# Optimization experiments

Hardware: AMD Instinct MI355X
Metric: run time of the kernel (lower is better)

The kernel has to match this reference:

```python
import jax, jax.numpy as jnp
import numpy as np

K = 10          # n_near
BN_EPS = 1e-5   # BatchNorm eps; running stats at init: mean=0, var=1


def knn_idx(xt, k):
    # xt: [b, n, c] -> [b, n, k] indices of k nearest (incl. self)
    sq = jnp.sum(xt * xt, axis=-1)                               # [b, n]
    d = sq[:, :, None] - 2.0 * jnp.einsum('bnc,bmc->bnm', xt, xt) + sq[:, None, :]
    return jax.lax.top_k(-d, k)[1]                               # [b, n, k]


def graph_feature(x, k):
    # x: [b, c, n] -> [b, 2c, n, k]  (DGCNN edge features)
    xt = x.transpose(0, 2, 1)                                    # [b, n, c]
    idx = knn_idx(xt, k)                                         # [b, n, k]
    nei = jnp.take_along_axis(xt[:, None, :, :], idx[..., None], axis=2)  # [b, n, k, c]
    cen = xt[:, :, None, :]                                      # [b, n, 1, c]
    feat = jnp.concatenate([nei - cen, jnp.broadcast_to(cen, nei.shape)], axis=-1)
    return feat.transpose(0, 3, 1, 2)                            # [b, 2c, n, k]


def conv_bn_act(x, w, b, g, t):
    # 1x1 conv (any spatial rank) + inference BatchNorm (mean=0, var=1) + GELU
    sh = (1, -1) + (1,) * (x.ndim - 2)
    y = jnp.einsum('oi,bi...->bo...', w, x) + b.reshape(sh)
    y = y * (g.reshape(sh) / jnp.sqrt(1.0 + BN_EPS)) + t.reshape(sh)
    return jax.nn.gelu(y)


def setup_inputs() -> dict:
    key = jax.random.key(0)
    ks = jax.random.split(key, 8)
    d = {'x': jax.random.normal(ks[0], (8, 64, 2048), jnp.float32)}
    dims = {'11': (152, 128), '12': (181, 152), '21': (430, 362),
            '22': (512, 430), '31': (595, 693), '32': (512, 595)}
    for i, (tag, (o, inp)) in enumerate(dims.items()):
        d['w' + tag] = jax.random.normal(jax.random.fold_in(key, i + 1), (o, inp), jnp.float32) * 0.02
        d['b' + tag] = jnp.zeros((o,), jnp.float32)
        d['g' + tag] = jnp.ones((o,), jnp.float32)
        d['t' + tag] = jnp.zeros((o,), jnp.float32)
    return d


def reference(x, w11, b11, g11, t11, w12, b12, g12, t12,
              w21, b21, g21, t21, w22, b22, g22, t22,
              w31, b31, g31, t31, w32, b32, g32, t32):
    f = graph_feature(x, K)                       # [b, 128, n, k]
    f = conv_bn_act(f, w11, b11, g11, t11)
    f = conv_bn_act(f, w12, b12, g12, t12)        # [b, 181, n, k]
    x1 = jnp.max(f, axis=-1)                      # [b, 181, n]
    f = graph_feature(x1, K)                      # [b, 362, n, k]
    f = conv_bn_act(f, w21, b21, g21, t21)
    f = conv_bn_act(f, w22, b22, g22, t22)        # [b, 512, n, k]
    x2 = jnp.max(f, axis=-1)                      # [b, 512, n]
    f = jnp.concatenate([x1, x2], axis=1)         # [b, 693, n]
    f = conv_bn_act(f, w31, b31, g31, t31)
    f = conv_bn_act(f, w32, b32, g32, t32)        # [b, 512, n]
    return f
```

## Files before the change

### kernel.cpp

```cpp
#include <hip/hip_runtime.h>


typedef float f4 __attribute__((ext_vector_type(4)));
typedef float f32x4 __attribute__((ext_vector_type(4)));
typedef short bf16x8 __attribute__((ext_vector_type(8)));

#define BNRSQ 0.9999950000374997f

__device__ __forceinline__ float gelu_f(float x){
  float a = 0.7978845608028654f * (x + 0.044715f * x * x * x);
  float e = __expf(2.0f * a);
  float t = 1.0f - 2.0f / (e + 1.0f);
  return 0.5f * x * (1.0f + t);
}

__device__ __forceinline__ short f2b(float x){
  unsigned u = __float_as_uint(x);
  unsigned r = (u + 0x7fffu + ((u >> 16) & 1u)) >> 16;
  return (short)r;
}
__device__ __forceinline__ float b2f(short s){
  return __uint_as_float(((unsigned)(unsigned short)s) << 16);
}

__global__ void makewt_k(const float* __restrict__ W, float* __restrict__ dst,
                         int O, int Cin, int Cpad, int ld, int split){
  int id = blockIdx.x * 256 + threadIdx.x;
  if (id >= Cpad * O) return;
  int c = id / O;
  int o = id - c * O;
  float v = 0.f;
  if (c < Cin){
    float w0 = W[(size_t)o * ld + c];
    v = split ? (W[(size_t)o * ld + Cin + c] - w0) : w0;
  }
  dst[id] = v;
}

__global__ void makew12r_k(const float* __restrict__ w12, float* __restrict__ Wr){
  int id = blockIdx.x * 256 + threadIdx.x;
  if (id >= 38 * 192 * 4) return;
  int i = id & 3;
  int c = (id >> 2) % 192;
  int kq = id / 768;
  int k = kq * 4 + i;
  float v = 0.f;
  if (c < 181 && k < 152) v = w12[(size_t)c * 152 + k];
  Wr[id] = v;
}

__global__ void makewsb_k(const float* __restrict__ W, short* __restrict__ dst){
  int n = blockIdx.x;
  int k = threadIdx.x;
  if (k >= 192) return;
  short v = 0;
  if (k < 181){
    if (n < 430) v = f2b(W[(size_t)n * 362 + k]);
    else if (n >= 448 && n < 878){
      int m = n - 448;
      v = f2b(W[(size_t)m * 362 + 181 + k] - W[(size_t)m * 362 + k]);
    }
  }
  dst[(size_t)n * 192 + k] = v;
}

__global__ void makewb_k(const float* __restrict__ W, short* __restrict__ dst,
                         int N, int K, int Kpad){
  int n = blockIdx.y;
  int k = blockIdx.x * 256 + threadIdx.x;
  if (k >= Kpad) return;
  short v = 0;
  if (n < N && k < K) v = f2b(W[(size_t)n * K + k]);
  dst[(size_t)n * Kpad + k] = v;
}

__global__ __launch_bounds__(256) void transpose_k(const float* __restrict__ x, float* __restrict__ xt){
  __shared__ float tile[64][65];
  int b = blockIdx.y;
  int n0 = blockIdx.x * 64;
  int t = threadIdx.x;
  int a = t & 63, r = t >> 6;
  #pragma unroll
  for (int s = 0; s < 16; s++){
    int c = r + s * 4;
    tile[c][a] = x[((size_t)b * 64 + c) * 2048 + n0 + a];
  }
  __syncthreads();
  #pragma unroll
  for (int s = 0; s < 16; s++){
    int n = r + s * 4;
    xt[((size_t)b * 2048 + n0 + n) * 64 + a] = tile[a][n];
  }
}

__global__ __launch_bounds__(256) void sqnorm_k(const float* __restrict__ X, float* __restrict__ sq,
                                                int C, int ld, int npts){
  int gid = blockIdx.x * blockDim.x + threadIdx.x;
  int wid = gid >> 6, lane = gid & 63;
  if (wid >= npts) return;
  const float* row = X + (size_t)wid * ld;
  float s = 0.f;
  for (int c = lane; c < C; c += 64){ float v = row[c]; s += v * v; }
  #pragma unroll
  for (int off = 32; off; off >>= 1) s += __shfl_xor(s, off);
  if (lane == 0) sq[wid] = s;
}

__global__ __launch_bounds__(256) void dist_k(const float* __restrict__ X, const float* __restrict__ sq,
                                              float* __restrict__ dist, int C, int ldx){
  __shared__ float As[16][132];
  __shared__ float Bs[16][132];
  const int z = blockIdx.z;
  const float* Xb = X + (size_t)z * 2048 * ldx;
  const float* sqb = sq + (z << 11);
  float* db = dist + (size_t)z * 2048 * 2048;
  const int i0 = blockIdx.y * 128, j0 = blockIdx.x * 128;
  const int t = threadIdx.x;
  const int ti = t >> 4, tj = t & 15;
  const int r = t & 127, q8 = (t >> 7) * 8;
  float acc[2][2][4][4];
  #pragma unroll
  for (int a = 0; a < 2; a++)
    #pragma unroll
    for (int b = 0; b < 2; b++)
      #pragma unroll
      for (int u = 0; u < 4; u++)
        #pragma unroll
        for (int v = 0; v < 4; v++) acc[a][b][u][v] = 0.f;
  const float* Ag = Xb + (size_t)(i0 + r) * ldx + q8;
  const float* Bg = Xb + (size_t)(j0 + r) * ldx + q8;
  for (int c0 = 0; c0 < C; c0 += 16){
    f4 av0 = *(const f4*)(Ag + c0);
    f4 av1 = *(const f4*)(Ag + c0 + 4);
    f4 bv0 = *(const f4*)(Bg + c0);
    f4 bv1 = *(const f4*)(Bg + c0 + 4);
    __syncthreads();
    #pragma unroll
    for (int i = 0; i < 4; i++){
      As[q8 + i][r] = av0[i];  As[q8 + 4 + i][r] = av1[i];
      Bs[q8 + i][r] = bv0[i];  Bs[q8 + 4 + i][r] = bv1[i];
    }
    __syncthreads();
    #pragma unroll
    for (int k = 0; k < 16; k++){
      f4 a0 = *(const f4*)&As[k][ti * 4];
      f4 a1 = *(const f4*)&As[k][ti * 4 + 64];
      f4 b0 = *(const f4*)&Bs[k][tj * 4];
      f4 b1 = *(const f4*)&Bs[k][tj * 4 + 64];
      #pragma unroll
      for (int u = 0; u < 4; u++)
        #pragma unroll
        for (int v = 0; v < 4; v++){
          acc[0][0][u][v] += a0[u] * b0[v];
          acc[0][1][u][v] += a0[u] * b1[v];
          acc[1][0][u][v] += a1[u] * b0[v];
          acc[1][1][u][v] += a1[u] * b1[v];
        }
    }
  }
  #pragma unroll
  for (int ia = 0; ia < 2; ia++){
    #pragma unroll
    for (int u = 0; u < 4; u++){
      int i = i0 + ia * 64 + ti * 4 + u;
      float si = sqb[i];
      #pragma unroll
      for (int jb = 0; jb < 2; jb++){
        int j = j0 + jb * 64 + tj * 4;
        f4 o;
        #pragma unroll
        for (int v = 0; v < 4; v++) o[v] = si + sqb[j + v] - 2.0f * acc[ia][jb][u][v];
        *(f4*)&db[(size_t)i * 2048 + j] = o;
      }
    }
  }
}

__global__ __launch_bounds__(256) void topk_k(const float* __restrict__ dist, int* __restrict__ idxout){
  int z = blockIdx.y;
  int lane = threadIdx.x & 63;
  int row = blockIdx.x * 4 + (threadIdx.x >> 6);
  const float* d = dist + (size_t)z * 2048 * 2048 + (size_t)row * 2048;
  float v[32];
  #pragma unroll
  for (int s = 0; s < 32; s++) v[s] = d[s * 64 + lane];
  int* outp = idxout + (size_t)z * 20480 + (size_t)row * 10;
  for (int it = 0; it < 10; ++it){
    float bv = 3.0e38f; int bi = 0x7fffffff;
    #pragma unroll
    for (int s = 0; s < 32; s++){
      if (v[s] < bv){ bv = v[s]; bi = s * 64 + lane; }
    }
    #pragma unroll
    for (int off = 32; off; off >>= 1){
      float ov = __shfl_xor(bv, off);
      int   oi = __shfl_xor(bi, off);
      if (ov < bv || (ov == bv && oi < bi)){ bv = ov; bi = oi; }
    }
    #pragma unroll
    for (int s = 0; s < 32; s++) if (s * 64 + lane == bi) v[s] = 3.0e38f;
    if (lane == 0) outp[it] = bi;
  }
}

__global__ __launch_bounds__(256) void yz_k(const float* __restrict__ Amat, int C,
                                            const float* __restrict__ B1, const float* __restrict__ B2,
                                            int O, float* __restrict__ Y, float* __restrict__ Z){
  __shared__ float As[16][68];
  __shared__ float B1s[16][68];
  __shared__ float B2s[16][68];
  int m0 = blockIdx.y * 64, o0 = blockIdx.x * 64;
  int t = threadIdx.x;
  int cc = t & 15, rr = t >> 4;
  int oo = t & 63, kk = t >> 6;
  float accY[4][4], accZ[4][4];
  #pragma unroll
  for (int u = 0; u < 4; u++)
    #pragma unroll
    for (int v = 0; v < 4; v++){ accY[u][v] = 0.f; accZ[u][v] = 0.f; }
  for (int c0 = 0; c0 < C; c0 += 16){
    #pragma unroll
    for (int u = 0; u < 4; u++){
      int ii = rr + u * 16;
      As[cc][ii] = ((c0 + cc) < C) ? Amat[(size_t)(m0 + ii) * C + c0 + cc] : 0.f;
    }
    #pragma unroll
    for (int u = 0; u < 4; u++){
      int c = kk * 4 + u;
      bool ok = ((c0 + c) < C) && ((o0 + oo) < O);
      B1s[c][oo] = ok ? B1[(size_t)(c0 + c) * O + o0 + oo] : 0.f;
      B2s[c][oo] = ok ? B2[(size_t)(c0 + c) * O + o0 + oo] : 0.f;
    }
    __syncthreads();
    #pragma unroll
    for (int k = 0; k < 16; k++){
      f4 a  = *(const f4*)&As[k][rr * 4];
      f4 b1 = *(const f4*)&B1s[k][cc * 4];
      f4 b2 = *(const f4*)&B2s[k][cc * 4];
      #pragma unroll
      for (int u = 0; u < 4; u++)
        #pragma unroll
        for (int v = 0; v < 4; v++){
          accY[u][v] += a[u] * b1[v];
          accZ[u][v] += a[u] * b2[v];
        }
    }
    __syncthreads();
  }
  #pragma unroll
  for (int u = 0; u < 4; u++){
    int m = m0 + rr * 4 + u;
    #pragma unroll
    for (int v = 0; v < 4; v++){
      int o = o0 + cc * 4 + v;
      if (o < O){
        Y[(size_t)m * O + o] = accY[u][v];
        Z[(size_t)m * O + o] = accZ[u][v];
      }
    }
  }
}

__global__ __launch_bounds__(256) void fused1_k(
    const float* __restrict__ Y1, const float* __restrict__ Z1,
    const int* __restrict__ idx, const float* __restrict__ Wr12,
    const float* __restrict__ bb11, const float* __restrict__ gg11, const float* __restrict__ tt11,
    const float* __restrict__ bb12, const float* __restrict__ gg12, const float* __restrict__ tt12,
    float* __restrict__ x1t){
  __shared__ float h1[80][152];
  __shared__ int sidx[80];
  const int n0 = blockIdx.x * 8;
  const int t = threadIdx.x;
  if (t < 80) sidx[t] = idx[(size_t)n0 * 10 + t];
  __syncthreads();
  const int base = (n0 >> 11) << 11;
  {
    const int tc = t & 63, tr = t >> 6;
    for (int c = tc; c < 152; c += 64){
      float bb = bb11[c], sc = gg11[c] * BNRSQ, tb = tt11[c];
      for (int r = tr; r < 80; r += 4){
        int p = r / 10;
        int j = base + sidx[r];
        float y = Y1[(size_t)j * 152 + c] + Z1[(size_t)(n0 + p) * 152 + c];
        h1[r][c] = gelu_f((y + bb) * sc + tb);
      }
    }
  }
  __syncthreads();
  const int p = t >> 5, kh = (t >> 4) & 1, cg = t & 15;
  const int rbase = p * 10 + kh * 5;
  float acc[5][12];
  #pragma unroll
  for (int k = 0; k < 5; k++)
    #pragma unroll
    for (int j = 0; j < 12; j++) acc[k][j] = 0.f;
  for (int kq = 0; kq < 38; kq++){
    const float* wp = Wr12 + ((size_t)kq * 192 + cg) * 4;
    f4 wv[12];
    #pragma unroll
    for (int j = 0; j < 12; j++) wv[j] = *(const f4*)(wp + j * 64);
    f4 hv[5];
    #pragma unroll
    for (int k = 0; k < 5; k++) hv[k] = *(const f4*)&h1[rbase + k][kq * 4];
    #pragma unroll
    for (int k = 0; k < 5; k++)
      #pragma unroll
      for (int j = 0; j < 12; j++)
        acc[k][j] += hv[k][0] * wv[j][0] + hv[k][1] * wv[j][1]
                   + hv[k][2] * wv[j][2] + hv[k][3] * wv[j][3];
  }
  #pragma unroll
  for (int j = 0; j < 12; j++){
    int c = cg + j * 16;
    float m = 0.f;
    if (c < 181){
      float bb = bb12[c], sc = gg12[c] * BNRSQ, tb = tt12[c];
      m = -3.0e38f;
      #pragma unroll
      for (int k = 0; k < 5; k++){
        float v = gelu_f((acc[k][j] + bb) * sc + tb);
        m = fmaxf(m, v);
      }
    }
    float o = __shfl_xor(m, 16);
    m = fmaxf(m, o);
    if (kh == 0) x1t[(size_t)(n0 + p) * 192 + c] = (c < 181) ? m : 0.f;
  }
}

__global__ __launch_bounds__(256) void castx1_k(const float* __restrict__ x1t, short* __restrict__ x1b){
  int id = blockIdx.x * 256 + threadIdx.x;
  f4 v = *(const f4*)&x1t[(size_t)id * 4];
  short4 o;
  o.x = f2b(v[0]); o.y = f2b(v[1]); o.z = f2b(v[2]); o.w = f2b(v[3]);
  *(short4*)&x1b[(size_t)id * 4] = o;
}

__global__ __launch_bounds__(256) void h2_k(
    const float* __restrict__ YZ, const int* __restrict__ idx,
    const float* __restrict__ bb21, const float* __restrict__ gg21, const float* __restrict__ tt21,
    short* __restrict__ H2){
  __shared__ int sidx[10];
  int p = blockIdx.x;
  int t = threadIdx.x;
  if (t < 10) sidx[t] = idx[(size_t)p * 10 + t];
  __syncthreads();
  int cA = t;
  int cB = t + 256;
  float zA = YZ[(size_t)p * 896 + 448 + cA] + bb21[cA];
  float scA = gg21[cA] * BNRSQ, tbA = tt21[cA];
  float zB = 0.f, scB = 0.f, tbB = 0.f;
  bool realB = cB < 430, padB = cB < 448;
  if (realB){
    zB = YZ[(size_t)p * 896 + 448 + cB] + bb21[cB];
    scB = gg21[cB] * BNRSQ; tbB = tt21[cB];
  }
  #pragma unroll
  for (int k = 0; k < 10; k++){
    int nb = sidx[k];
    size_t rb = ((size_t)p * 10 + k) * 448;
    float yA = YZ[(size_t)nb * 896 + cA] + zA;
    H2[rb + cA] = f2b(gelu_f(yA * scA + tbA));
    if (padB){
      short v = 0;
      if (realB){
        float yB = YZ[(size_t)nb * 896 + cB] + zB;
        v = f2b(gelu_f(yB * scB + tbB));
      }
      H2[rb + cB] = v;
    }
  }
}

template<int MODE>
__global__ __launch_bounds__(256) void gemm_k(const short* __restrict__ A,
                                              const short* __restrict__ Bt,
                                              int Kp, int Nld, int Nreal,
                                              const float* __restrict__ bv,
                                              const float* __restrict__ gv,
                                              const float* __restrict__ tv,
                                              void* __restrict__ outp){
  __shared__ short As[128][40];
  __shared__ short Bs[128][40];
  const int t = threadIdx.x;
  const int w = t >> 6, l = t & 63;
  const int m0 = blockIdx.y * 128, n0 = blockIdx.x * 128;
  f32x4 acc[2][8];
  #pragma unroll
  for (int i = 0; i < 2; i++)
    #pragma unroll
    for (int j = 0; j < 8; j++) acc[i][j] = (f32x4)0.f;
  const int ar = t >> 2, akc = t & 3;
  const short* Ag0 = A + (size_t)(m0 + ar) * Kp + akc * 8;
  const short* Ag1 = A + (size_t)(m0 + 64 + ar) * Kp + akc * 8;
  const short* Bg0 = Bt + (size_t)(n0 + ar) * Kp + akc * 8;
  const short* Bg1 = Bt + (size_t)(n0 + 64 + ar) * Kp + akc * 8;
  const int mrow = w * 32 + (l & 15);
  const int kg = (l >> 4) * 8;
  const int cl = l & 15;
  for (int k0 = 0; k0 < Kp; k0 += 32){
    int4 va0 = *(const int4*)(Ag0 + k0);
    int4 va1 = *(const int4*)(Ag1 + k0);
    int4 vb0 = *(const int4*)(Bg0 + k0);
    int4 vb1 = *(const int4*)(Bg1 + k0);
    __syncthreads();
    *(int4*)&As[ar][akc * 8]      = va0;
    *(int4*)&As[ar + 64][akc * 8] = va1;
    *(int4*)&Bs[ar][akc * 8]      = vb0;
    *(int4*)&Bs[ar + 64][akc * 8] = vb1;
    __syncthreads();
    bf16x8 a0 = *(const bf16x8*)&As[mrow][kg];
    bf16x8 a1 = *(const bf16x8*)&As[mrow + 16][kg];
    #pragma unroll
    for (int ni = 0; ni < 8; ni++){
      bf16x8 b = *(const bf16x8*)&Bs[cl + ni * 16][kg];
      acc[0][ni] = __builtin_amdgcn_mfma_f32_16x16x32_bf16(a0, b, acc[0][ni], 0, 0, 0);
      acc[1][ni] = __builtin_amdgcn_mfma_f32_16x16x32_bf16(a1, b, acc[1][ni], 0, 0, 0);
    }
  }
  const int rbase = (l >> 4) * 4;
  #pragma unroll
  for (int ni = 0; ni < 8; ni++){
    int n = n0 + ni * 16 + cl;
    float bb = 0.f, sc = 0.f, tb = 0.f;
    if (MODE != 2 && n < Nreal){ bb = bv[n]; sc = gv[n] * BNRSQ; tb = tv[n]; }
    #pragma unroll
    for (int mi = 0; mi < 2; mi++){
      #pragma unroll
      for (int r = 0; r < 4; r++){
        int m = m0 + w * 32 + mi * 16 + rbase + r;
        float a = acc[mi][ni][r];
        float v = (MODE == 2) ? a : gelu_f((a + bb) * sc + tb);
        if (MODE == 0) ((short*)outp)[(size_t)m * Nld + n] = f2b(v);
        else           ((float*)outp)[(size_t)m * Nld + n] = v;
      }
    }
  }
}

__global__ __launch_bounds__(256) void kmax_k(const short* __restrict__ Pb, float* __restrict__ x2t){
  int p = blockIdx.x;
  int t = threadIdx.x;
  #pragma unroll
  for (int j = 0; j < 2; j++){
    int o = t + j * 256;
    float m = -3.0e38f;
    #pragma unroll
    for (int k = 0; k < 10; k++) m = fmaxf(m, b2f(Pb[((size_t)p * 10 + k) * 512 + o]));
    x2t[(size_t)p * 512 + o] = m;
  }
}

__global__ __launch_bounds__(256) void fcat_k(const float* __restrict__ x1t, const float* __restrict__ x2t,
                                              short* __restrict__ F){
  size_t g = blockIdx.x;
  int t = threadIdx.x;
  for (int c = t; c < 704; c += 256){
    short v = 0;
    if (c < 181) v = f2b(x1t[g * 192 + c]);
    else if (c < 693) v = f2b(x2t[g * 512 + (c - 181)]);
    F[g * 704 + c] = v;
  }
}

__global__ __launch_bounds__(256) void trout_k(const float* __restrict__ H6, float* __restrict__ out){
  __shared__ float tile[64][65];
  int b = blockIdx.z;
  int nc = blockIdx.x * 64, oc = blockIdx.y * 64;
  int t = threadIdx.x;
  int a = t & 63, r = t >> 6;
  #pragma unroll
  for (int s = 0; s < 16; s++){
    int nl = r + s * 4;
    tile[nl][a] = H6[((size_t)b * 2048 + nc + nl) * 512 + oc + a];
  }
  __syncthreads();
  #pragma unroll
  for (int s = 0; s < 16; s++){
    int ol = r + s * 4;
    out[((size_t)(b * 512 + oc + ol)) * 2048 + nc + a] = tile[a][ol];
  }
}

extern "C" void kernel_launch(void* const* d_in, const int* in_sizes, int n_in,
                              void* d_out, int out_size, void* d_ws, size_t ws_size,
                              hipStream_t stream) {
  const float* x   = (const float*)d_in[0];
  const float* w11 = (const float*)d_in[1];
  const float* b11 = (const float*)d_in[2];
  const float* g11 = (const float*)d_in[3];
  const float* t11 = (const float*)d_in[4];
  const float* w12 = (const float*)d_in[5];
  const float* b12 = (const float*)d_in[6];
  const float* g12 = (const float*)d_in[7];
  const float* t12 = (const float*)d_in[8];
  const float* w21 = (const float*)d_in[9];
  const float* b21 = (const float*)d_in[10];
  const float* g21 = (const float*)d_in[11];
  const float* t21 = (const float*)d_in[12];
  const float* w22 = (const float*)d_in[13];
  const float* b22 = (const float*)d_in[14];
  const float* g22 = (const float*)d_in[15];
  const float* t22 = (const float*)d_in[16];
  const float* w31 = (const float*)d_in[17];
  const float* b31 = (const float*)d_in[18];
  const float* g31 = (const float*)d_in[19];
  const float* t31 = (const float*)d_in[20];
  const float* w32 = (const float*)d_in[21];
  const float* b32 = (const float*)d_in[22];
  const float* g32 = (const float*)d_in[23];
  const float* t32 = (const float*)d_in[24];
  float* out = (float*)d_out;
  char* ws = (char*)d_ws;

  size_t off = 0;
  auto alloc = [&](size_t nbytes) -> char* {
    char* p = ws + off;
    off += ((nbytes + 255) & ~(size_t)255);
    return p;
  };
  float* x1t  = (float*)alloc((size_t)16384 * 192 * 4);
  short* x1b  = (short*)alloc((size_t)16384 * 192 * 2);
  float* x2t  = (float*)alloc((size_t)16384 * 512 * 4);
  float* sq1  = (float*)alloc(65536);
  float* sq2  = (float*)alloc(65536);
  int*   idx1 = (int*)  alloc(655360);
  int*   idx2 = (int*)  alloc(655360);
  float* WaT11 = (float*)alloc(64 * 152 * 4);
  float* WdT11 = (float*)alloc(64 * 152 * 4);
  float* Wr12  = (float*)alloc(38 * 192 * 4 * 4);
  short* W21sb = (short*)alloc((size_t)896 * 192 * 2);
  short* W22b  = (short*)alloc((size_t)512 * 448 * 2);
  short* W31b  = (short*)alloc((size_t)640 * 704 * 2);
  short* W32b  = (short*)alloc((size_t)512 * 640 * 2);
  char* arena = ws + off;
  const size_t ARENA = 80216064;
  if (off + ARENA > ws_size) return;
  float* distP = (float*)(arena);
  float* xt    = (float*)(arena + 33554432);
  float* Y1    = (float*)(arena + 37748736);
  float* Z1    = (float*)(arena + 47710208);
  short* H2b   = (short*)(arena + 33554432);
  short* Pb    = (short*)(arena + 51904512);
  float* YZ2   = (float*)(arena + 72876032);
  short* F     = (short*)(arena);
  short* H5    = (short*)(arena + 23068672);
  float* H6    = (float*)(arena + 44040192);

  auto mk = [&](const float* W, float* dst, int O, int Cin, int Cpad, int ld, int split){
    int n = Cpad * O;
    makewt_k<<<dim3((n + 255) / 256), dim3(256), 0, stream>>>(W, dst, O, Cin, Cpad, ld, split);
  };
  mk(w11, WaT11, 152, 64, 64, 128, 0);
  mk(w11, WdT11, 152, 64, 64, 128, 1);
  makew12r_k<<<dim3(114), dim3(256), 0, stream>>>(w12, Wr12);
  makewsb_k<<<dim3(896), dim3(256), 0, stream>>>(w21, W21sb);
  makewb_k<<<dim3(2, 512), dim3(256), 0, stream>>>(w22, W22b, 512, 430, 448);
  makewb_k<<<dim3(3, 640), dim3(256), 0, stream>>>(w31, W31b, 595, 693, 704);
  makewb_k<<<dim3(3, 512), dim3(256), 0, stream>>>(w32, W32b, 512, 595, 640);

  transpose_k<<<dim3(32, 8), dim3(256), 0, stream>>>(x, xt);
  sqnorm_k<<<dim3(4096), dim3(256), 0, stream>>>(xt, sq1, 64, 64, 16384);

  for (int pb = 0; pb < 4; pb++){
    dist_k<<<dim3(16, 16, 2), dim3(256), 0, stream>>>(xt + (size_t)pb * 2 * 2048 * 64,
                                                      sq1 + pb * 4096, distP, 64, 64);
    topk_k<<<dim3(512, 2), dim3(256), 0, stream>>>(distP, idx1 + (size_t)pb * 2 * 20480);
  }
  yz_k<<<dim3(3, 256), dim3(256), 0, stream>>>(xt, 64, WaT11, WdT11, 152, Y1, Z1);
  fused1_k<<<dim3(2048), dim3(256), 0, stream>>>(Y1, Z1, idx1, Wr12,
                                                 b11, g11, t11, b12, g12, t12, x1t);
  castx1_k<<<dim3(3072), dim3(256), 0, stream>>>(x1t, x1b);
  sqnorm_k<<<dim3(4096), dim3(256), 0, stream>>>(x1t, sq2, 192, 192, 16384);

  for (int pb = 0; pb < 4; pb++){
    dist_k<<<dim3(16, 16, 2), dim3(256), 0, stream>>>(x1t + (size_t)pb * 2 * 2048 * 192,
                                                      sq2 + pb * 4096, distP, 192, 192);
    topk_k<<<dim3(512, 2), dim3(256), 0, stream>>>(distP, idx2 + (size_t)pb * 2 * 20480);
    for (int q = 0; q < 2; q++){
      int b = pb * 2 + q;
      gemm_k<2><<<dim3(7, 16), dim3(256), 0, stream>>>(x1b + (size_t)b * 2048 * 192, W21sb,
                                                       192, 896, 896,
                                                       nullptr, nullptr, nullptr, (void*)YZ2);
      h2_k<<<dim3(2048), dim3(256), 0, stream>>>(YZ2, idx2 + (size_t)b * 20480,
                                                 b21, g21, t21, H2b);
      gemm_k<0><<<dim3(4, 160), dim3(256), 0, stream>>>(H2b, W22b, 448, 512, 512,
                                                        b22, g22, t22, (void*)Pb);
      kmax_k<<<dim3(2048), dim3(256), 0, stream>>>(Pb, x2t + (size_t)b * 2048 * 512);
    }
  }

  fcat_k<<<dim3(16384), dim3(256), 0, stream>>>(x1t, x2t, F);
  gemm_k<0><<<dim3(5, 128), dim3(256), 0, stream>>>(F, W31b, 704, 640, 595,
                                                    b31, g31, t31, (void*)H5);
  gemm_k<1><<<dim3(4, 128), dim3(256), 0, stream>>>(H5, W32b, 640, 512, 512,
                                                    b32, g32, t32, (void*)H6);
  trout_k<<<dim3(32, 8, 8), dim3(256), 0, stream>>>(H6, out);
}
```

Before: 1.232 ms.

## Batch kNN and edge-conv stages over larger groups, store x2 in bf16

Raises the per-launch batch for the distance/top-k and second-stage conv chain from 1–2 to 2–4 batches, rearranging workspace buffers to fit the larger intermediates. This cuts the number of kernel launches and gives each launch a bigger grid. h2_k now adds the per-batch base offset to the neighbour indices so one launch can span two batches. x2 is written directly as bf16 by kmax_k, so fcat_k reads half the bytes and does no conversion. fused1_k also gets a min-blocks occupancy hint, which may raise register pressure.

```diff
diff --git a/kernel.cpp b/kernel.cpp
--- a/kernel.cpp
+++ b/kernel.cpp
@@ -261,7 +261,7 @@
   }
 }
 
-__global__ __launch_bounds__(256) void fused1_k(
+__global__ __launch_bounds__(256, 3) void fused1_k(
     const float* __restrict__ Y1, const float* __restrict__ Z1,
     const int* __restrict__ idx, const float* __restrict__ Wr12,
     const float* __restrict__ bb11, const float* __restrict__ gg11, const float* __restrict__ tt11,
@@ -341,24 +341,24 @@
     const float* __restrict__ bb21, const float* __restrict__ gg21, const float* __restrict__ tt21,
     short* __restrict__ H2){
   __shared__ int sidx[10];
-  int p = blockIdx.x;
+  int bl = blockIdx.x;
   int t = threadIdx.x;
-  if (t < 10) sidx[t] = idx[(size_t)p * 10 + t];
+  if (t < 10) sidx[t] = ((bl >> 11) << 11) + idx[(size_t)bl * 10 + t];
   __syncthreads();
   int cA = t;
   int cB = t + 256;
-  float zA = YZ[(size_t)p * 896 + 448 + cA] + bb21[cA];
+  float zA = YZ[(size_t)bl * 896 + 448 + cA] + bb21[cA];
   float scA = gg21[cA] * BNRSQ, tbA = tt21[cA];
   float zB = 0.f, scB = 0.f, tbB = 0.f;
   bool realB = cB < 430, padB = cB < 448;
   if (realB){
-    zB = YZ[(size_t)p * 896 + 448 + cB] + bb21[cB];
+    zB = YZ[(size_t)bl * 896 + 448 + cB] + bb21[cB];
     scB = gg21[cB] * BNRSQ; tbB = tt21[cB];
   }
   #pragma unroll
   for (int k = 0; k < 10; k++){
     int nb = sidx[k];
-    size_t rb = ((size_t)p * 10 + k) * 448;
+    size_t rb = ((size_t)bl * 10 + k) * 448;
     float yA = YZ[(size_t)nb * 896 + cA] + zA;
     H2[rb + cA] = f2b(gelu_f(yA * scA + tbA));
     if (padB){
@@ -438,7 +438,7 @@
   }
 }
 
-__global__ __launch_bounds__(256) void kmax_k(const short* __restrict__ Pb, float* __restrict__ x2t){
+__global__ __launch_bounds__(256) void kmax_k(const short* __restrict__ Pb, short* __restrict__ x2b){
   int p = blockIdx.x;
   int t = threadIdx.x;
   #pragma unroll
@@ -447,18 +447,18 @@
     float m = -3.0e38f;
     #pragma unroll
     for (int k = 0; k < 10; k++) m = fmaxf(m, b2f(Pb[((size_t)p * 10 + k) * 512 + o]));
-    x2t[(size_t)p * 512 + o] = m;
-  }
-}
-
-__global__ __launch_bounds__(256) void fcat_k(const float* __restrict__ x1t, const float* __restrict__ x2t,
+    x2b[(size_t)p * 512 + o] = f2b(m);
+  }
+}
+
+__global__ __launch_bounds__(256) void fcat_k(const float* __restrict__ x1t, const short* __restrict__ x2b,
                                               short* __restrict__ F){
   size_t g = blockIdx.x;
   int t = threadIdx.x;
   for (int c = t; c < 704; c += 256){
     short v = 0;
     if (c < 181) v = f2b(x1t[g * 192 + c]);
-    else if (c < 693) v = f2b(x2t[g * 512 + (c - 181)]);
+    else if (c < 693) v = x2b[g * 512 + (c - 181)];
     F[g * 704 + c] = v;
   }
 }
@@ -521,7 +521,7 @@
   };
   float* x1t  = (float*)alloc((size_t)16384 * 192 * 4);
   short* x1b  = (short*)alloc((size_t)16384 * 192 * 2);
-  float* x2t  = (float*)alloc((size_t)16384 * 512 * 4);
+  short* x2b  = (short*)alloc((size_t)16384 * 512 * 2);
   float* sq1  = (float*)alloc(65536);
   float* sq2  = (float*)alloc(65536);
   int*   idx1 = (int*)  alloc(655360);
@@ -534,15 +534,15 @@
   short* W31b  = (short*)alloc((size_t)640 * 704 * 2);
   short* W32b  = (short*)alloc((size_t)512 * 640 * 2);
   char* arena = ws + off;
-  const size_t ARENA = 80216064;
+  const size_t ARENA = 93323264;
   if (off + ARENA > ws_size) return;
   float* distP = (float*)(arena);
-  float* xt    = (float*)(arena + 33554432);
-  float* Y1    = (float*)(arena + 37748736);
-  float* Z1    = (float*)(arena + 47710208);
-  short* H2b   = (short*)(arena + 33554432);
-  short* Pb    = (short*)(arena + 51904512);
-  float* YZ2   = (float*)(arena + 72876032);
+  float* Y1    = (float*)(arena + 67108864);
+  float* Z1    = (float*)(arena + 77070336);
+  float* xt    = (float*)(arena + 87031808);
+  short* Pb    = (short*)(arena);
+  short* H2b   = (short*)(arena + 41943040);
+  float* YZ2g  = (float*)(arena + 78643200);
   short* F     = (short*)(arena);
   short* H5    = (short*)(arena + 23068672);
   float* H6    = (float*)(arena + 44040192);
@@ -562,10 +562,10 @@
   transpose_k<<<dim3(32, 8), dim3(256), 0, stream>>>(x, xt);
   sqnorm_k<<<dim3(4096), dim3(256), 0, stream>>>(xt, sq1, 64, 64, 16384);
 
-  for (int pb = 0; pb < 4; pb++){
-    dist_k<<<dim3(16, 16, 2), dim3(256), 0, stream>>>(xt + (size_t)pb * 2 * 2048 * 64,
-                                                      sq1 + pb * 4096, distP, 64, 64);
-    topk_k<<<dim3(512, 2), dim3(256), 0, stream>>>(distP, idx1 + (size_t)pb * 2 * 20480);
+  for (int pb = 0; pb < 2; pb++){
+    dist_k<<<dim3(16, 16, 4), dim3(256), 0, stream>>>(xt + (size_t)pb * 4 * 2048 * 64,
+                                                      sq1 + pb * 8192, distP, 64, 64);
+    topk_k<<<dim3(512, 4), dim3(256), 0, stream>>>(distP, idx1 + (size_t)pb * 4 * 20480);
   }
   yz_k<<<dim3(3, 256), dim3(256), 0, stream>>>(xt, 64, WaT11, WdT11, 152, Y1, Z1);
   fused1_k<<<dim3(2048), dim3(256), 0, stream>>>(Y1, Z1, idx1, Wr12,
@@ -573,24 +573,23 @@
   castx1_k<<<dim3(3072), dim3(256), 0, stream>>>(x1t, x1b);
   sqnorm_k<<<dim3(4096), dim3(256), 0, stream>>>(x1t, sq2, 192, 192, 16384);
 
-  for (int pb = 0; pb < 4; pb++){
-    dist_k<<<dim3(16, 16, 2), dim3(256), 0, stream>>>(x1t + (size_t)pb * 2 * 2048 * 192,
-                                                      sq2 + pb * 4096, distP, 192, 192);
-    topk_k<<<dim3(512, 2), dim3(256), 0, stream>>>(distP, idx2 + (size_t)pb * 2 * 20480);
-    for (int q = 0; q < 2; q++){
-      int b = pb * 2 + q;
-      gemm_k<2><<<dim3(7, 16), dim3(256), 0, stream>>>(x1b + (size_t)b * 2048 * 192, W21sb,
-                                                       192, 896, 896,
-                                                       nullptr, nullptr, nullptr, (void*)YZ2);
-      h2_k<<<dim3(2048), dim3(256), 0, stream>>>(YZ2, idx2 + (size_t)b * 20480,
-                                                 b21, g21, t21, H2b);
-      gemm_k<0><<<dim3(4, 160), dim3(256), 0, stream>>>(H2b, W22b, 448, 512, 512,
-                                                        b22, g22, t22, (void*)Pb);
-      kmax_k<<<dim3(2048), dim3(256), 0, stream>>>(Pb, x2t + (size_t)b * 2048 * 512);
-    }
-  }
-
-  fcat_k<<<dim3(16384), dim3(256), 0, stream>>>(x1t, x2t, F);
+  for (int pb = 0; pb < 2; pb++){
+    dist_k<<<dim3(16, 16, 4), dim3(256), 0, stream>>>(x1t + (size_t)pb * 4 * 2048 * 192,
+                                                      sq2 + pb * 8192, distP, 192, 192);
+    topk_k<<<dim3(512, 4), dim3(256), 0, stream>>>(distP, idx2 + (size_t)pb * 4 * 20480);
+  }
+  for (int g = 0; g < 4; g++){
+    gemm_k<2><<<dim3(7, 32), dim3(256), 0, stream>>>(x1b + (size_t)g * 4096 * 192, W21sb,
+                                                     192, 896, 896,
+                                                     nullptr, nullptr, nullptr, (void*)YZ2g);
+    h2_k<<<dim3(4096), dim3(256), 0, stream>>>(YZ2g, idx2 + (size_t)g * 40960,
+                                               b21, g21, t21, H2b);
+    gemm_k<0><<<dim3(4, 320), dim3(256), 0, stream>>>(H2b, W22b, 448, 512, 512,
+                                                      b22, g22, t22, (void*)Pb);
+    kmax_k<<<dim3(4096), dim3(256), 0, stream>>>(Pb, x2b + (size_t)g * 4096 * 512);
+  }
+
+  fcat_k<<<dim3(16384), dim3(256), 0, stream>>>(x1t, x2b, F);
   gemm_k<0><<<dim3(5, 128), dim3(256), 0, stream>>>(F, W31b, 704, 640, 595,
                                                     b31, g31, t31, (void*)H5);
   gemm_k<1><<<dim3(4, 128), dim3(256), 0, stream>>>(H5, W32b, 640, 512, 512,
```

Measured after the change: 1.355 ms. 10.0% more time.
